# Kernel optimization log

Measured on AMD Instinct MI355X. Metric: run time of the kernel, lower is better.

Reference implementation:

```python
import jax, jax.numpy as jnp
import numpy as np
from jax import lax

B, CIN, COUT, H, W = 8, 128, 128, 128, 128
HID = COUT // 2  # expansion 0.5
K = 3            # kernel size
PAD = 1


def silu(v):
    return v * jax.nn.sigmoid(v)


def base_conv1x1(x, w, s, b):
    # 1x1 conv (no bias) + folded-BN affine (scale s, bias b) + SiLU
    y = jnp.einsum('bchw,oc->bohw', x, w)
    return silu(y * s[None, :, None, None] + b[None, :, None, None])


def bilinear_gather(img, py, px):
    Hin, Win = img.shape[1], img.shape[2]
    y0 = jnp.floor(py)
    x0 = jnp.floor(px)
    wy = py - y0
    wx = px - x0

    def corner(yc, xc):
        valid = (yc >= 0) & (yc <= Hin - 1) & (xc >= 0) & (xc <= Win - 1)
        yi = jnp.clip(yc, 0, Hin - 1).astype(jnp.int32)
        xi = jnp.clip(xc, 0, Win - 1).astype(jnp.int32)
        v = img[:, yi, xi]  # [C, Kk, H, W]
        return v * valid[None].astype(img.dtype)

    v00 = corner(y0, x0)
    v01 = corner(y0, x0 + 1)
    v10 = corner(y0 + 1, x0)
    v11 = corner(y0 + 1, x0 + 1)
    wy = wy[None]
    wx = wx[None]
    return (v00 * (1 - wy) * (1 - wx) + v01 * (1 - wy) * wx
            + v10 * wy * (1 - wx) + v11 * wy * wx)


def deform_conv_depthwise(x, off_w, off_b, dw):
    # x: [B, C, H, W]; off_w: [2*K*K, C, 3, 3]; dw: [C, K, K] (depthwise, groups=C)
    b, c, h, w = x.shape
    off = lax.conv_general_dilated(
        x, off_w, window_strides=(1, 1), padding=((PAD, PAD), (PAD, PAD)),
        dimension_numbers=('NCHW', 'OIHW', 'NCHW'))
    off = off + off_b[None, :, None, None]
    off = off.reshape(b, K * K, 2, h, w)  # torchvision: (dy, dx) per tap
    dy, dx = off[:, :, 0], off[:, :, 1]   # [B, 9, H, W]

    ky = jnp.repeat(jnp.arange(K, dtype=x.dtype), K)  # [9]
    kx = jnp.tile(jnp.arange(K, dtype=x.dtype), K)
    yy = jnp.arange(h, dtype=x.dtype)[None, :, None]  # [1, H, 1]
    xx = jnp.arange(w, dtype=x.dtype)[None, None, :]
    py = yy + ky[:, None, None] - PAD  # [9, H, W]
    px = xx + kx[:, None, None] - PAD
    py = py[None] + dy  # [B, 9, H, W]
    px = px[None] + dx

    sampled = jax.vmap(bilinear_gather)(x, py, px)  # [B, C, 9, H, W]
    return jnp.einsum('bckhw,ck->bchw', sampled, dw.reshape(c, K * K))


def setup_inputs() -> dict:
    key = jax.random.key(0)
    ks = jax.random.split(key, 12)
    f = jnp.float32
    inp = {
        'x': jax.random.normal(ks[0], (B, CIN, H, W), f),
        'w1': jax.random.normal(ks[1], (HID, CIN), f) * 0.05,
        's1': jnp.ones((HID,), f), 'b1': jnp.zeros((HID,), f),
        'w2': jax.random.normal(ks[2], (HID, CIN), f) * 0.05,
        's2': jnp.ones((HID,), f), 'b2': jnp.zeros((HID,), f),
        'w3': jax.random.normal(ks[3], (COUT, 2 * HID), f) * 0.05,
        's3': jnp.ones((COUT,), f), 'b3': jnp.zeros((COUT,), f),
        'off_w': jax.random.normal(ks[4], (2 * K * K, HID, K, K), f) * 0.01,
        'off_b': jnp.zeros((2 * K * K,), f),
        'dw': jax.random.normal(ks[5], (HID, K, K), f) * 0.1,
    }
    return inp


def reference(x, w1, s1, b1, w2, s2, b2, w3, s3, b3, off_w, off_b, dw):
    x1 = base_conv1x1(x, w1, s1, b1)          # [B, HID, H, W]
    x2 = base_conv1x1(x, w2, s2, b2)          # [B, HID, H, W]
    x1 = deform_conv_depthwise(x1, off_w, off_b, dw)
    xc = jnp.concatenate([x1, x2], axis=1)    # [B, 2*HID, H, W]
    return base_conv1x1(xc, w3, s3, b3)       # [B, COUT, H, W]
```

## Files before the change

### kernel.cpp

```cpp
#include <hip/hip_runtime.h>

typedef unsigned short u16;
typedef unsigned int   u32;
typedef unsigned char  u8;

#define BB    8
#define CINC  128
#define HIDC  64
#define COUTC 128
#define HH    128
#define WWD   128
#define HWN   16384
#define NPOS  (BB*HWN)

typedef __attribute__((ext_vector_type(8))) short bf16x8;
typedef __attribute__((ext_vector_type(4))) float f32x4;

__device__ __forceinline__ float b2f(u16 u){
    union { u32 i; float f; } v; v.i = ((u32)u) << 16; return v.f;
}
__device__ __forceinline__ u16 f2b(float f){
    union { float f; u32 i; } v; v.f = f;
    u32 i = v.i;
    i += 0x7fffu + ((i >> 16) & 1u);
    return (u16)(i >> 16);
}
__device__ __forceinline__ float blo(u32 u){
    union { u32 i; float f; } v; v.i = u << 16; return v.f;
}
__device__ __forceinline__ float bhi(u32 u){
    union { u32 i; float f; } v; v.i = u & 0xFFFF0000u; return v.f;
}
__device__ __forceinline__ float silu(float y){
    return y / (1.f + __expf(-y));
}

template<bool ISB>
__device__ __forceinline__ float ldp(const void* p, int i){
    if (ISB) return b2f(((const u16*)p)[i]);
    return ((const float*)p)[i];
}

template<bool ISB>
__device__ __forceinline__ void k0_body(
    const void* w1, const void* s1, const void* b1,
    const void* w2, const void* s2, const void* b2,
    const void* w3, const void* s3, const void* b3,
    const void* offw, const void* offb, const void* dw,
    u16* __restrict__ wbc, u16* __restrict__ wb3,
    float* __restrict__ bfc, float* __restrict__ bf3,
    u16* __restrict__ wA, float* __restrict__ ob32, float* __restrict__ dwfT)
{
    int t = blockIdx.x*256 + threadIdx.x;
    if (t < 8192){
        wbc[t] = f2b(ldp<ISB>(w1,t) * ldp<ISB>(s1,t>>7));
    } else if (t < 16384){
        int u = t - 8192;
        wbc[t] = f2b(ldp<ISB>(w2,u) * ldp<ISB>(s2,u>>7));
    }
    if (t < 16384){
        wb3[t] = f2b(ldp<ISB>(w3,t) * ldp<ISB>(s3,t>>7));
    }
    if (t < 18432){
        int set  = t / 9216, rem = t % 9216;
        int tap  = rem / 1024; int rem2 = rem % 1024;
        int chunk= rem2 >> 9;  int rem3 = rem2 & 511;
        int lane = rem3 >> 3;  int jp   = rem3 & 7;
        int jg   = set*16 + (lane & 15);
        int c    = chunk*32 + (lane>>4)*8 + jp;
        float v  = (jg < 18) ? ldp<ISB>(offw, (jg*HIDC + c)*9 + tap) : 0.f;
        wA[t] = f2b(v);
    }
    if (t < HIDC)  bfc[t]      = ldp<ISB>(b1,t);
    if (t >= HIDC && t < 2*HIDC) bfc[t] = ldp<ISB>(b2,t-HIDC);
    if (t < COUTC) bf3[t] = ldp<ISB>(b3,t);
    if (t < 32)    ob32[t] = (t < 18) ? ldp<ISB>(offb,t) : 0.f;
    if (t < HIDC*9){
        int c = t / 9, k = t % 9;
        dwfT[k*HIDC + c] = ldp<ISB>(dw,t);
    }
}

__global__ __launch_bounds__(256) void k0_prep(
    const void* w1, const void* s1, const void* b1,
    const void* w2, const void* s2, const void* b2,
    const void* w3, const void* s3, const void* b3,
    const void* offw, const void* offb, const void* dw,
    u16* wbc, u16* wb3, float* bfc, float* bf3,
    u16* wA, float* ob32, float* dwfT)
{
    bool isb = (((const u32*)s1)[0] == 0x3F803F80u);
    if (isb) k0_body<true >(w1,s1,b1,w2,s2,b2,w3,s3,b3,offw,offb,dw,wbc,wb3,bfc,bf3,wA,ob32,dwfT);
    else     k0_body<false>(w1,s1,b1,w2,s2,b2,w3,s3,b3,offw,offb,dw,wbc,wb3,bfc,bf3,wA,ob32,dwfT);
}

template<bool ISB>
__device__ __forceinline__ void k1_body(const void* __restrict__ xv,
    const u16* __restrict__ wbc, const float* __restrict__ bfc,
    u16* __restrict__ x1, u16* __restrict__ x2, u8* __restrict__ sx8)
{
    const int posb = blockIdx.x*64;
    const int bidx = posb >> 14;
    const int hwb  = posb & (HWN-1);

    {
        const int R  = threadIdx.x >> 2;
        const int qq = threadIdx.x & 3;
        u32* dst = (u32*)(sx8 + R*272 + qq*64);
        if (ISB){
            const u16* r0 = (const u16*)xv + (size_t)bidx*CINC*HWN + (size_t)(2*R)*HWN + hwb + qq*16;
            const u16* r1 = r0 + HWN;
            uint4 a0 = *(const uint4*)(r0);
            uint4 a1 = *(const uint4*)(r0 + 8);
            uint4 c0 = *(const uint4*)(r1);
            uint4 c1 = *(const uint4*)(r1 + 8);
            u32 A[8] = {a0.x,a0.y,a0.z,a0.w,a1.x,a1.y,a1.z,a1.w};
            u32 C[8] = {c0.x,c0.y,c0.z,c0.w,c1.x,c1.y,c1.z,c1.w};
            #pragma unroll
            for (int k = 0; k < 8; ++k){
                dst[2*k]   = (A[k] & 0xFFFFu) | (C[k] << 16);
                dst[2*k+1] = (A[k] >> 16)     | (C[k] & 0xFFFF0000u);
            }
        } else {
            const float* r0 = (const float*)xv + (size_t)bidx*CINC*HWN + (size_t)(2*R)*HWN + hwb + qq*16;
            const float* r1 = r0 + HWN;
            #pragma unroll
            for (int k = 0; k < 8; ++k){
                float2 f0 = *(const float2*)(r0 + 2*k);
                float2 f1 = *(const float2*)(r1 + 2*k);
                dst[2*k]   = (u32)f2b(f0.x) | ((u32)f2b(f1.x) << 16);
                dst[2*k+1] = (u32)f2b(f0.y) | ((u32)f2b(f1.y) << 16);
            }
        }
    }
    __syncthreads();

    const int w    = threadIdx.x >> 6;
    const int lane = threadIdx.x & 63;
    const int n    = lane & 15;
    const int quad = lane >> 4;

    bf16x8 wf[2][4];
    #pragma unroll
    for (int m = 0; m < 2; ++m)
        #pragma unroll
        for (int t = 0; t < 4; ++t)
            wf[m][t] = *(const bf16x8*)(wbc + (size_t)(w*32 + m*16 + n)*CINC + t*32 + quad*8);

    f32x4 acc[2][4];
    #pragma unroll
    for (int m = 0; m < 2; ++m)
        #pragma unroll
        for (int s = 0; s < 4; ++s) acc[m][s] = (f32x4){0.f,0.f,0.f,0.f};

    #pragma unroll
    for (int t = 0; t < 4; ++t){
        #pragma unroll
        for (int sub = 0; sub < 4; ++sub){
            union { u32 u[4]; bf16x8 v; } bb;
            #pragma unroll
            for (int jp = 0; jp < 4; ++jp)
                bb.u[jp] = *(const u32*)(sx8 + (t*16 + quad*4 + jp)*272 + (sub*16 + n)*4);
            acc[0][sub] = __builtin_amdgcn_mfma_f32_16x16x32_bf16(wf[0][t], bb.v, acc[0][sub], 0,0,0);
            acc[1][sub] = __builtin_amdgcn_mfma_f32_16x16x32_bf16(wf[1][t], bb.v, acc[1][sub], 0,0,0);
        }
    }

    #pragma unroll
    for (int m = 0; m < 2; ++m){
        const int ob = w*32 + m*16 + quad*4;
        float4 bi = *(const float4*)(bfc + ob);
        u16* dbuf = (ob < 64) ? x1 : x2;
        const int oo = ob & 63;
        #pragma unroll
        for (int sub = 0; sub < 4; ++sub){
            const u32 lo = (u32)f2b(silu(acc[m][sub][0] + bi.x))
                         | ((u32)f2b(silu(acc[m][sub][1] + bi.y)) << 16);
            const u32 hi = (u32)f2b(silu(acc[m][sub][2] + bi.z))
                         | ((u32)f2b(silu(acc[m][sub][3] + bi.w)) << 16);
            *(uint2*)(dbuf + (size_t)(posb + sub*16 + n)*HIDC + oo) = make_uint2(lo, hi);
        }
    }
}

__global__ __launch_bounds__(256) void k1_mfma(const void* x, const u32* s1probe,
    const u16* wbc, const float* bfc, u16* x1, u16* x2)
{
    __shared__ __align__(16) u8 sx8[64*272];
    bool isb = (s1probe[0] == 0x3F803F80u);
    if (isb) k1_body<true >(x, wbc, bfc, x1, x2, sx8);
    else     k1_body<false>(x, wbc, bfc, x1, x2, sx8);
}

__global__ __launch_bounds__(256) void k23_fused(const u16* __restrict__ x1,
    const u16* __restrict__ wA, const float* __restrict__ ob32,
    const float* __restrict__ dwfT, u16* __restrict__ x1d)
{
    __shared__ float s_dwf[576];
    __shared__ float s_offs[64*21];
    __shared__ int   s_offi[64*12];
    __shared__ __align__(16) float4 s_facs[64*9];

    const int tid  = threadIdx.x;
    if (tid < 144)
        *(float4*)(s_dwf + tid*4) = *(const float4*)(dwfT + tid*4);

    const int w    = tid >> 6;
    const int lane = tid & 63;
    const int n    = lane & 15;
    const int quad = lane >> 4;
    const int posb = blockIdx.x*64;
    const int b    = posb >> 14;
    const u16* bbase = x1 + (size_t)b*HWN*HIDC;

    {
        const int posbase = posb + w*16;
        const int hw  = posbase & (HWN-1);
        const int y   = hw >> 7;
        const int x0  = hw & (WWD-1);
        const int xb  = x0 + n - 1;

        f32x4 acc0 = (f32x4){0.f,0.f,0.f,0.f};
        f32x4 acc1 = (f32x4){0.f,0.f,0.f,0.f};

        #pragma unroll
        for (int ky = 0; ky < 3; ++ky){
            int ys = y + ky - 1;
            if ((unsigned)ys >= HH) continue;
            const u16* rowp = bbase + (size_t)ys*WWD*HIDC;
            #pragma unroll
            for (int kx = 0; kx < 3; ++kx){
                int  xs  = xb + kx;
                int  xcl = min(max(xs, 0), WWD-1);
                bool vx  = ((unsigned)xs < WWD);
                const int tap = ky*3 + kx;
                #pragma unroll
                for (int ch = 0; ch < 2; ++ch){
                    bf16x8 bfr = *(const bf16x8*)(rowp + xcl*HIDC + ch*32 + quad*8);
                    if (!vx) bfr = (bf16x8){0,0,0,0,0,0,0,0};
                    bf16x8 a0 = *(const bf16x8*)(wA + ((0*9 + tap)*2 + ch)*512 + lane*8);
                    bf16x8 a1 = *(const bf16x8*)(wA + ((1*9 + tap)*2 + ch)*512 + lane*8);
                    acc0 = __builtin_amdgcn_mfma_f32_16x16x32_bf16(a0, bfr, acc0, 0,0,0);
                    acc1 = __builtin_amdgcn_mfma_f32_16x16x32_bf16(a1, bfr, acc1, 0,0,0);
                }
            }
        }
        const int pl = w*16 + n;
        #pragma unroll
        for (int r = 0; r < 4; ++r){
            int j0 = quad*4 + r;
            s_offs[pl*21 + j0] = acc0[r] + ob32[j0];
            int j1 = 16 + quad*4 + r;
            if (j1 < 18)
                s_offs[pl*21 + j1] = acc1[r] + ob32[j1];
        }
    }
    __syncthreads();

    for (int task = tid; task < 576; task += 256){
        int pl = task / 9;
        int k  = task - pl*9;
        int pos = posb + pl;
        int hw = pos & (HWN-1);
        int y  = hw >> 7, x = hw & (WWD-1);
        float dy = s_offs[pl*21 + 2*k];
        float dx = s_offs[pl*21 + 2*k + 1];
        float py = (float)(y + k/3 - 1) + dy;
        float px = (float)(x + k%3 - 1) + dx;
        float fy = floorf(py), fx = floorf(px);
        float wy = py - fy,    wx = px - fx;
        int y0 = (int)fy, x0i = (int)fx;
        float vy0 = ((unsigned)y0      < HH)  ? 1.f : 0.f;
        float vy1 = ((unsigned)(y0+1)  < HH)  ? 1.f : 0.f;
        float vx0 = ((unsigned)x0i     < WWD) ? 1.f : 0.f;
        float vx1 = ((unsigned)(x0i+1) < WWD) ? 1.f : 0.f;
        int yc0 = min(max(y0,   0), HH-1),  yc1 = min(max(y0+1, 0), HH-1);
        int xc0 = min(max(x0i,  0), WWD-1), xc1 = min(max(x0i+1, 0), WWD-1);
        float wy1 = 1.f - wy, wx1 = 1.f - wx;
        float4 w4;
        w4.x = wy1*wx1*vy0*vx0;
        w4.y = wy1*wx *vy0*vx1;
        w4.z = wy *wx1*vy1*vx0;
        w4.w = wy *wx *vy1*vx1;
        int o0 = (yc0*WWD + xc0)*HIDC;
        int sx = (xc1 != xc0) ? 1 : 0;
        int sy = (yc1 != yc0) ? 1 : 0;
        s_offi[pl*12 + k] = o0 | (sx<<20) | (sy<<21);
        s_facs[pl*9 + k]  = w4;
    }
    __syncthreads();

    const int cg = lane & 7;
    const u32* xb32 = (const u32*)bbase + cg*4;
    #pragma unroll
    for (int it = 0; it < 2; ++it){
        const int posl = w*16 + it*8 + (lane >> 3);
        const int pos  = posb + posl;
        float acc[8];
        #pragma unroll
        for (int j = 0; j < 8; ++j) acc[j] = 0.f;
        #pragma unroll
        for (int k = 0; k < 9; ++k){
            const int    pk = s_offi[posl*12 + k];
            const float4 f  = s_facs[posl*9 + k];
            const float4 d0 = *(const float4*)(s_dwf + k*HIDC + cg*8);
            const float4 d1 = *(const float4*)(s_dwf + k*HIDC + cg*8 + 4);
            const int o0  = (pk & 0xFFFFF) >> 1;
            const int dxs = (pk & (1<<20)) ? (HIDC>>1)       : 0;
            const int dys = (pk & (1<<21)) ? ((WWD*HIDC)>>1) : 0;
            const uint4 q00 = *(const uint4*)(xb32 + o0);
            const uint4 q01 = *(const uint4*)(xb32 + o0 + dxs);
            const uint4 q10 = *(const uint4*)(xb32 + o0 + dys);
            const uint4 q11 = *(const uint4*)(xb32 + o0 + dys + dxs);
            #define BIL(J, C00, C01, C10, C11, DLO, DHI) { \
                float slo = blo(C00)*f.x + blo(C01)*f.y + blo(C10)*f.z + blo(C11)*f.w; \
                float shi = bhi(C00)*f.x + bhi(C01)*f.y + bhi(C10)*f.z + bhi(C11)*f.w; \
                acc[2*(J)]   += slo*(DLO); \
                acc[2*(J)+1] += shi*(DHI); }
            BIL(0, q00.x, q01.x, q10.x, q11.x, d0.x, d0.y)
            BIL(1, q00.y, q01.y, q10.y, q11.y, d0.z, d0.w)
            BIL(2, q00.z, q01.z, q10.z, q11.z, d1.x, d1.y)
            BIL(3, q00.w, q01.w, q10.w, q11.w, d1.z, d1.w)
            #undef BIL
        }
        const u32 r0 = (u32)f2b(acc[0]) | ((u32)f2b(acc[1]) << 16);
        const u32 r1 = (u32)f2b(acc[2]) | ((u32)f2b(acc[3]) << 16);
        const u32 r2 = (u32)f2b(acc[4]) | ((u32)f2b(acc[5]) << 16);
        const u32 r3 = (u32)f2b(acc[6]) | ((u32)f2b(acc[7]) << 16);
        *(uint4*)(x1d + (size_t)pos*HIDC + cg*8) = make_uint4(r0, r1, r2, r3);
    }
}

template<bool ISB>
__device__ __forceinline__ void k4_body(const u16* __restrict__ x1d,
    const u16* __restrict__ x2,
    const u16* __restrict__ wb3, const float* __restrict__ bf3,
    void* __restrict__ out)
{
    const int posb = blockIdx.x*64;
    const int bidx = posb >> 14;
    const int hwb  = posb & (HWN-1);
    const int w    = threadIdx.x >> 6;
    const int lane = threadIdx.x & 63;
    const int n    = lane & 15;
    const int quad = lane >> 4;

    bf16x8 wf[2][4];
    #pragma unroll
    for (int m = 0; m < 2; ++m)
        #pragma unroll
        for (int t = 0; t < 4; ++t)
            wf[m][t] = *(const bf16x8*)(wb3 + (size_t)(w*32 + m*16 + n)*CINC + t*32 + quad*8);

    f32x4 acc[2][4];
    #pragma unroll
    for (int m = 0; m < 2; ++m)
        #pragma unroll
        for (int s = 0; s < 4; ++s) acc[m][s] = (f32x4){0.f,0.f,0.f,0.f};

    #pragma unroll
    for (int t = 0; t < 4; ++t){
        const u16* src = (t < 2) ? x1d : x2;
        #pragma unroll
        for (int sub = 0; sub < 4; ++sub){
            bf16x8 bfr = *(const bf16x8*)(src + (size_t)(posb + sub*16 + n)*HIDC + (t&1)*32 + quad*8);
            acc[0][sub] = __builtin_amdgcn_mfma_f32_16x16x32_bf16(wf[0][t], bfr, acc[0][sub], 0,0,0);
            acc[1][sub] = __builtin_amdgcn_mfma_f32_16x16x32_bf16(wf[1][t], bfr, acc[1][sub], 0,0,0);
        }
    }

    u16*   ob16 = (u16*)  out + (size_t)bidx*COUTC*HWN + hwb;
    float* obf  = (float*)out + (size_t)bidx*COUTC*HWN + hwb;
    #pragma unroll
    for (int m = 0; m < 2; ++m){
        const int ob = w*32 + m*16 + quad*4;
        float4 bi = *(const float4*)(bf3 + ob);
        #pragma unroll
        for (int sub = 0; sub < 4; ++sub){
            const int pp = sub*16 + n;
            #pragma unroll
            for (int r = 0; r < 4; ++r){
                const float bv = (r==0)?bi.x:(r==1)?bi.y:(r==2)?bi.z:bi.w;
                const float v = silu(acc[m][sub][r] + bv);
                if (ISB) ob16[(size_t)(ob+r)*HWN + pp] = f2b(v);
                else     obf [(size_t)(ob+r)*HWN + pp] = v;
            }
        }
    }
}

__global__ __launch_bounds__(256) void k4_mfma(const u16* x1d, const u16* x2,
    const u32* s1probe, const u16* wb3, const float* bf3, void* out)
{
    bool isb = (s1probe[0] == 0x3F803F80u);
    if (isb) k4_body<true >(x1d, x2, wb3, bf3, out);
    else     k4_body<false>(x1d, x2, wb3, bf3, out);
}

extern "C" void kernel_launch(void* const* d_in, const int* in_sizes, int n_in,
                              void* d_out, int out_size, void* d_ws, size_t ws_size,
                              hipStream_t stream)
{
    const void* x    = d_in[0];
    const void* w1   = d_in[1];
    const void* s1   = d_in[2];
    const void* b1   = d_in[3];
    const void* w2   = d_in[4];
    const void* s2   = d_in[5];
    const void* b2   = d_in[6];
    const void* w3   = d_in[7];
    const void* s3   = d_in[8];
    const void* b3   = d_in[9];
    const void* offw = d_in[10];
    const void* offb = d_in[11];
    const void* dw   = d_in[12];

    char* ws = (char*)d_ws;
    u16*   x1    = (u16*)  (ws + 0);
    u16*   x2    = (u16*)  (ws + 16777216);
    u16*   x1d   = (u16*)  (ws + 33554432);
    u16*   wbc   = (u16*)  (ws + 59768832);
    u16*   wb3   = (u16*)  (ws + 59801600);
    u16*   wA    = (u16*)  (ws + 59834368);
    float* dwfT  = (float*)(ws + 59871232);
    float* bfc   = (float*)(ws + 59873536);
    float* bf3   = (float*)(ws + 59874048);
    float* ob32  = (float*)(ws + 59874560);

    k0_prep<<<72, 256, 0, stream>>>(w1,s1,b1, w2,s2,b2, w3,s3,b3, offw,offb,dw,
                                    wbc, wb3, bfc, bf3, wA, ob32, dwfT);
    k1_mfma  <<<NPOS/64, 256, 0, stream>>>(x, (const u32*)s1, wbc, bfc, x1, x2);
    k23_fused<<<NPOS/64, 256, 0, stream>>>(x1, wA, ob32, dwfT, x1d);
    k4_mfma  <<<NPOS/64, 256, 0, stream>>>(x1d, x2, (const u32*)s1, wb3, bf3, d_out);
}
```

Before: 227.4 us.

## Fuse deformable depthwise conv with final 1x1 conv via shared memory

Merges the deformable-conv kernel and the final 1x1 MFMA conv into one kernel. The deformed x1 tile is written to padded LDS instead of a global intermediate buffer, then read back as MFMA B-fragments. This removes a 16 MB global write and read plus one kernel launch. In exchange it raises LDS use per block, which may lower occupancy, and adds a block-wide sync before the GEMM phase.

```diff
diff --git a/kernel.cpp b/kernel.cpp
--- a/kernel.cpp
+++ b/kernel.cpp
@@ -192,15 +192,15 @@
     else     k1_body<false>(x, wbc, bfc, x1, x2, sx8);
 }
 
-__global__ __launch_bounds__(256) void k23_fused(const u16* __restrict__ x1,
+template<bool ISB>
+__device__ __forceinline__ void k234_body(const u16* __restrict__ x1,
+    const u16* __restrict__ x2,
     const u16* __restrict__ wA, const float* __restrict__ ob32,
-    const float* __restrict__ dwfT, u16* __restrict__ x1d)
-{
-    __shared__ float s_dwf[576];
-    __shared__ float s_offs[64*21];
-    __shared__ int   s_offi[64*12];
-    __shared__ __align__(16) float4 s_facs[64*9];
-
+    const float* __restrict__ dwfT,
+    const u16* __restrict__ wb3, const float* __restrict__ bf3,
+    void* __restrict__ out,
+    float* s_dwf, float* s_offs, int* s_offi, float4* s_facs, u16* s_x1d)
+{
     const int tid  = threadIdx.x;
     if (tid < 144)
         *(float4*)(s_dwf + tid*4) = *(const float4*)(dwfT + tid*4);
@@ -211,6 +211,7 @@
     const int quad = lane >> 4;
     const int posb = blockIdx.x*64;
     const int b    = posb >> 14;
+    const int hwb  = posb & (HWN-1);
     const u16* bbase = x1 + (size_t)b*HWN*HIDC;
 
     {
@@ -295,7 +296,6 @@
     #pragma unroll
     for (int it = 0; it < 2; ++it){
         const int posl = w*16 + it*8 + (lane >> 3);
-        const int pos  = posb + posl;
         float acc[8];
         #pragma unroll
         for (int j = 0; j < 8; ++j) acc[j] = 0.f;
@@ -327,74 +327,73 @@
         const u32 r1 = (u32)f2b(acc[2]) | ((u32)f2b(acc[3]) << 16);
         const u32 r2 = (u32)f2b(acc[4]) | ((u32)f2b(acc[5]) << 16);
         const u32 r3 = (u32)f2b(acc[6]) | ((u32)f2b(acc[7]) << 16);
-        *(uint4*)(x1d + (size_t)pos*HIDC + cg*8) = make_uint4(r0, r1, r2, r3);
-    }
-}
-
-template<bool ISB>
-__device__ __forceinline__ void k4_body(const u16* __restrict__ x1d,
-    const u16* __restrict__ x2,
-    const u16* __restrict__ wb3, const float* __restrict__ bf3,
-    void* __restrict__ out)
-{
-    const int posb = blockIdx.x*64;
-    const int bidx = posb >> 14;
-    const int hwb  = posb & (HWN-1);
-    const int w    = threadIdx.x >> 6;
-    const int lane = threadIdx.x & 63;
-    const int n    = lane & 15;
-    const int quad = lane >> 4;
-
-    bf16x8 wf[2][4];
-    #pragma unroll
-    for (int m = 0; m < 2; ++m)
-        #pragma unroll
-        for (int t = 0; t < 4; ++t)
-            wf[m][t] = *(const bf16x8*)(wb3 + (size_t)(w*32 + m*16 + n)*CINC + t*32 + quad*8);
-
-    f32x4 acc[2][4];
-    #pragma unroll
-    for (int m = 0; m < 2; ++m)
-        #pragma unroll
-        for (int s = 0; s < 4; ++s) acc[m][s] = (f32x4){0.f,0.f,0.f,0.f};
-
-    #pragma unroll
-    for (int t = 0; t < 4; ++t){
-        const u16* src = (t < 2) ? x1d : x2;
-        #pragma unroll
-        for (int sub = 0; sub < 4; ++sub){
-            bf16x8 bfr = *(const bf16x8*)(src + (size_t)(posb + sub*16 + n)*HIDC + (t&1)*32 + quad*8);
-            acc[0][sub] = __builtin_amdgcn_mfma_f32_16x16x32_bf16(wf[0][t], bfr, acc[0][sub], 0,0,0);
-            acc[1][sub] = __builtin_amdgcn_mfma_f32_16x16x32_bf16(wf[1][t], bfr, acc[1][sub], 0,0,0);
-        }
-    }
-
-    u16*   ob16 = (u16*)  out + (size_t)bidx*COUTC*HWN + hwb;
-    float* obf  = (float*)out + (size_t)bidx*COUTC*HWN + hwb;
-    #pragma unroll
-    for (int m = 0; m < 2; ++m){
-        const int ob = w*32 + m*16 + quad*4;
-        float4 bi = *(const float4*)(bf3 + ob);
-        #pragma unroll
-        for (int sub = 0; sub < 4; ++sub){
-            const int pp = sub*16 + n;
-            #pragma unroll
-            for (int r = 0; r < 4; ++r){
-                const float bv = (r==0)?bi.x:(r==1)?bi.y:(r==2)?bi.z:bi.w;
-                const float v = silu(acc[m][sub][r] + bv);
-                if (ISB) ob16[(size_t)(ob+r)*HWN + pp] = f2b(v);
-                else     obf [(size_t)(ob+r)*HWN + pp] = v;
+        *(uint4*)(s_x1d + posl*88 + cg*8) = make_uint4(r0, r1, r2, r3);
+    }
+    __syncthreads();
+
+    {
+        bf16x8 wf[2][4];
+        #pragma unroll
+        for (int m = 0; m < 2; ++m)
+            #pragma unroll
+            for (int t = 0; t < 4; ++t)
+                wf[m][t] = *(const bf16x8*)(wb3 + (size_t)(w*32 + m*16 + n)*CINC + t*32 + quad*8);
+
+        f32x4 acc[2][4];
+        #pragma unroll
+        for (int m = 0; m < 2; ++m)
+            #pragma unroll
+            for (int s = 0; s < 4; ++s) acc[m][s] = (f32x4){0.f,0.f,0.f,0.f};
+
+        #pragma unroll
+        for (int t = 0; t < 4; ++t){
+            #pragma unroll
+            for (int sub = 0; sub < 4; ++sub){
+                bf16x8 bfr;
+                if (t < 2)
+                    bfr = *(const bf16x8*)(s_x1d + (sub*16 + n)*88 + (t&1)*32 + quad*8);
+                else
+                    bfr = *(const bf16x8*)(x2 + (size_t)(posb + sub*16 + n)*HIDC + (t&1)*32 + quad*8);
+                acc[0][sub] = __builtin_amdgcn_mfma_f32_16x16x32_bf16(wf[0][t], bfr, acc[0][sub], 0,0,0);
+                acc[1][sub] = __builtin_amdgcn_mfma_f32_16x16x32_bf16(wf[1][t], bfr, acc[1][sub], 0,0,0);
             }
         }
-    }
-}
-
-__global__ __launch_bounds__(256) void k4_mfma(const u16* x1d, const u16* x2,
-    const u32* s1probe, const u16* wb3, const float* bf3, void* out)
-{
+
+        u16*   ob16 = (u16*)  out + (size_t)b*COUTC*HWN + hwb;
+        float* obf  = (float*)out + (size_t)b*COUTC*HWN + hwb;
+        #pragma unroll
+        for (int m = 0; m < 2; ++m){
+            const int ob = w*32 + m*16 + quad*4;
+            float4 bi = *(const float4*)(bf3 + ob);
+            #pragma unroll
+            for (int sub = 0; sub < 4; ++sub){
+                const int pp = sub*16 + n;
+                #pragma unroll
+                for (int r = 0; r < 4; ++r){
+                    const float bv = (r==0)?bi.x:(r==1)?bi.y:(r==2)?bi.z:bi.w;
+                    const float v = silu(acc[m][sub][r] + bv);
+                    if (ISB) ob16[(size_t)(ob+r)*HWN + pp] = f2b(v);
+                    else     obf [(size_t)(ob+r)*HWN + pp] = v;
+                }
+            }
+        }
+    }
+}
+
+__global__ __launch_bounds__(256) void k234_fused(const u16* x1, const u16* x2,
+    const u32* s1probe, const u16* wA, const float* ob32, const float* dwfT,
+    const u16* wb3, const float* bf3, void* out)
+{
+    __shared__ float s_dwf[576];
+    __shared__ float s_offs[64*21];
+    __shared__ int   s_offi[64*12];
+    __shared__ __align__(16) float4 s_facs[64*9];
+    __shared__ __align__(16) u16 s_x1d[64*88];
     bool isb = (s1probe[0] == 0x3F803F80u);
-    if (isb) k4_body<true >(x1d, x2, wb3, bf3, out);
-    else     k4_body<false>(x1d, x2, wb3, bf3, out);
+    if (isb) k234_body<true >(x1, x2, wA, ob32, dwfT, wb3, bf3, out,
+                              s_dwf, s_offs, s_offi, s_facs, s_x1d);
+    else     k234_body<false>(x1, x2, wA, ob32, dwfT, wb3, bf3, out,
+                              s_dwf, s_offs, s_offi, s_facs, s_x1d);
 }
 
 extern "C" void kernel_launch(void* const* d_in, const int* in_sizes, int n_in,
@@ -418,7 +417,6 @@
     char* ws = (char*)d_ws;
     u16*   x1    = (u16*)  (ws + 0);
     u16*   x2    = (u16*)  (ws + 16777216);
-    u16*   x1d   = (u16*)  (ws + 33554432);
     u16*   wbc   = (u16*)  (ws + 59768832);
     u16*   wb3   = (u16*)  (ws + 59801600);
     u16*   wA    = (u16*)  (ws + 59834368);
@@ -429,7 +427,7 @@
 
     k0_prep<<<72, 256, 0, stream>>>(w1,s1,b1, w2,s2,b2, w3,s3,b3, offw,offb,dw,
                                     wbc, wb3, bfc, bf3, wA, ob32, dwfT);
-    k1_mfma  <<<NPOS/64, 256, 0, stream>>>(x, (const u32*)s1, wbc, bfc, x1, x2);
-    k23_fused<<<NPOS/64, 256, 0, stream>>>(x1, wA, ob32, dwfT, x1d);
-    k4_mfma  <<<NPOS/64, 256, 0, stream>>>(x1d, x2, (const u32*)s1, wb3, bf3, d_out);
-}
+    k1_mfma   <<<NPOS/64, 256, 0, stream>>>(x, (const u32*)s1, wbc, bfc, x1, x2);
+    k234_fused<<<NPOS/64, 256, 0, stream>>>(x1, x2, (const u32*)s1, wA, ob32,
+                                            dwfT, wb3, bf3, d_out);
+}
```

After: 244.0 us. 7.3% more time.
